# Optimization experiments

Hardware: AMD Instinct MI355X
Metric: run time of the kernel (lower is better)

The kernel has to match this reference:

```python
import jax, jax.numpy as jnp
import numpy as np

FP8_MAX = 448.0   # max normal of float8_e4m3fn
BLOCK = 128       # block_size
EPS = 1e-12


def setup_inputs() -> dict:
    key = jax.random.key(0)
    k1, k2 = jax.random.split(key)
    M, K, N = 8192, 2048, 2048  # tokens, in_features, out_features
    x = jax.random.normal(k1, (M, K), dtype=jnp.float32)
    # Build an fp8 blockwise-quantized weight (as the module stores it):
    w = jax.random.normal(k2, (N, K), dtype=jnp.float32) * 0.02
    wb = w.reshape(N // BLOCK, BLOCK, K // BLOCK, BLOCK)
    amax = jnp.max(jnp.abs(wb), axis=(1, 3))                      # [Nb, Kb]
    w_scale = jnp.maximum(amax, EPS) / FP8_MAX                    # fp32 per-block scale
    w_q = (wb / w_scale[:, None, :, None]).astype(jnp.float8_e4m3fn)
    weight = w_q.reshape(N, K)                                    # fp8 [N, K]
    return {"x": x, "weight": weight, "w_scale": w_scale}


def reference(x, weight, w_scale):
    M, K = x.shape
    N = weight.shape[0]
    # --- fp8_blockwise_act_quant: per (1, BLOCK) block along last dim ---
    xb = x.reshape(M, K // BLOCK, BLOCK)
    amax = jnp.max(jnp.abs(xb), axis=-1)                          # [M, Kb]
    x_scale = jnp.maximum(amax, EPS) / FP8_MAX                    # [M, Kb]
    x_q = (xb / x_scale[:, :, None]).astype(jnp.float8_e4m3fn).astype(jnp.float32)
    # --- blockwise_fp8_gemm: y[m,n] = sum_kb (xq_blk . wq_blk) * xs[m,kb] * ws[nb,kb]
    # Scales factor per-block, so dequantize then a single GEMM is exactly equivalent.
    x_deq = (x_q * x_scale[:, :, None]).reshape(M, K)             # [M, K]
    ws_full = jnp.repeat(jnp.repeat(w_scale, BLOCK, axis=0), BLOCK, axis=1)  # [N, K]
    w_deq = weight.astype(jnp.float32) * ws_full                  # [N, K]
    y = x_deq @ w_deq.T                                           # [M, N]
    return y
```

## Files before the change

kernel.cpp:

```cpp
#include <hip/hip_runtime.h>
#include <cstdint>
#include <cstddef>

#define MDIM 8192
#define KDIM 2048
#define NDIM 2048
#define QBLK 128
#define KB   (KDIM / QBLK)
#define NB   (NDIM / QBLK)

typedef float floatx4 __attribute__((ext_vector_type(4)));
typedef int   int4v   __attribute__((ext_vector_type(4)));
typedef int   int8v   __attribute__((ext_vector_type(8)));

#define AS1 __attribute__((address_space(1)))
#define AS3 __attribute__((address_space(3)))

__device__ inline float e4m3_rne(float q) {
    float aq = fabsf(q);
    float r;
    if (aq < 0.015625f) {
        r = rintf(aq * 512.0f) * 0.001953125f;
    } else {
        unsigned u = __float_as_uint(aq);
        unsigned rem = u & 0xFFFFFu;
        unsigned base = u & ~0xFFFFFu;
        unsigned inc = (rem > 0x80000u || (rem == 0x80000u && (u & 0x100000u))) ? 0x100000u : 0u;
        r = __uint_as_float(base + inc);
    }
    return q < 0.0f ? -r : r;
}

__device__ inline unsigned e4m3_encode(float r) {
    unsigned u = __float_as_uint(r);
    unsigned s = (u >> 24) & 0x80u;
    float a = fabsf(r);
    if (a < 0.015625f) return s | (unsigned)(a * 512.0f + 0.25f);
    unsigned e = ((u >> 23) & 0xFFu) - 120u;
    unsigned m = (u >> 20) & 7u;
    return s | (e << 3) | m;
}

__device__ inline float e4m3_decode(unsigned b) {
    unsigned s = b >> 7, e = (b >> 3) & 0xFu, m = b & 7u;
    float v;
    if (e == 0) v = (float)m * 0.001953125f;
    else        v = __uint_as_float((e + 120u) << 23) * (float)(8 + m) * 0.125f;
    return s ? -v : v;
}

__device__ inline int is_expbyte(unsigned b) {
    unsigned e = b & 0x7Fu;
    return (e >= 0x3Bu && e <= 0x43u) || e == 0x00u;
}

#define XQ_OFF  0
#define WQ_OFF  ((size_t)MDIM * KDIM)
#define XS_OFF  (WQ_OFF + (size_t)NDIM * KDIM)
#define FL_OFF  (XS_OFF + (size_t)MDIM * KB * 4)

#define QXB ((MDIM * KB) / 8)
#define DWB ((NDIM * KDIM / 8) / 256)

__global__ __launch_bounds__(256) void prep_kernel(const float* __restrict__ x,
                                                   const void* __restrict__ wq,
                                                   unsigned char* __restrict__ xq,
                                                   unsigned char* __restrict__ wq8,
                                                   float* __restrict__ xs,
                                                   int* __restrict__ flag) {
    const int tid = threadIdx.x;
    if (blockIdx.x == 0 && tid == 0) *flag = 0;

    if (blockIdx.x < QXB) {
        const int g = tid >> 5;
        const int l = tid & 31;
        const size_t bi = (size_t)blockIdx.x * 8 + g;
        const size_t base = bi << 7;

        const float4 v = *(const float4*)(x + base + (size_t)l * 4);
        float a = fmaxf(fmaxf(fabsf(v.x), fabsf(v.y)), fmaxf(fabsf(v.z), fabsf(v.w)));
        a = fmaxf(a, __shfl_xor(a, 1));
        a = fmaxf(a, __shfl_xor(a, 2));
        a = fmaxf(a, __shfl_xor(a, 4));
        a = fmaxf(a, __shfl_xor(a, 8));
        a = fmaxf(a, __shfl_xor(a, 16));

        const float scale = fmaxf(a, 1e-12f) / 448.0f;
        if (l == 0) xs[bi] = scale;

        const float q0 = v.x / scale, q1 = v.y / scale;
        const float q2 = v.z / scale, q3 = v.w / scale;
        int w = __builtin_amdgcn_cvt_pk_fp8_f32(q0, q1, 0, false);
        w = __builtin_amdgcn_cvt_pk_fp8_f32(q2, q3, w, true);
        *(unsigned*)(xq + base + (size_t)l * 4) = (unsigned)w;
    } else {
        const int lane = tid & 63;
        const unsigned pw = ((const unsigned*)wq)[lane];
        const unsigned long long m3 = __ballot(is_expbyte((pw >> 24) & 0xFFu));
        const unsigned long long m1 = __ballot(((pw >> 8) & 0xFFu) == 0u);
        const int f = (__popcll(m3) >= 56) ? ((__popcll(m1) >= 56) ? 2 : 1) : 0;

        const size_t idx = (size_t)(blockIdx.x - QXB) * 256 + tid;
        const size_t off = idx * 8;

        unsigned lo, hi;
        if (f == 2) {
            const float4* p = (const float4*)((const float*)wq + off);
            const float4 a = p[0], b = p[1];
            lo = e4m3_encode(a.x) | (e4m3_encode(a.y) << 8) | (e4m3_encode(a.z) << 16) | (e4m3_encode(a.w) << 24);
            hi = e4m3_encode(b.x) | (e4m3_encode(b.y) << 8) | (e4m3_encode(b.z) << 16) | (e4m3_encode(b.w) << 24);
        } else if (f == 1) {
            const ushort4 h0 = *(const ushort4*)((const unsigned short*)wq + off);
            const ushort4 h1 = *(((const ushort4*)((const unsigned short*)wq + off)) + 1);
            lo = e4m3_encode(__uint_as_float((unsigned)h0.x << 16))
               | (e4m3_encode(__uint_as_float((unsigned)h0.y << 16)) << 8)
               | (e4m3_encode(__uint_as_float((unsigned)h0.z << 16)) << 16)
               | (e4m3_encode(__uint_as_float((unsigned)h0.w << 16)) << 24);
            hi = e4m3_encode(__uint_as_float((unsigned)h1.x << 16))
               | (e4m3_encode(__uint_as_float((unsigned)h1.y << 16)) << 8)
               | (e4m3_encode(__uint_as_float((unsigned)h1.z << 16)) << 16)
               | (e4m3_encode(__uint_as_float((unsigned)h1.w << 16)) << 24);
        } else {
            const uint2 d = *(const uint2*)((const unsigned char*)wq + off);
            lo = d.x; hi = d.y;
        }
        *(uint2*)(wq8 + off) = make_uint2(lo, hi);
    }
}

__global__ __launch_bounds__(512, 2) void gemm_mx_kernel(const unsigned char* __restrict__ Aq,
                                                         const unsigned char* __restrict__ Bq,
                                                         const float* __restrict__ xs,
                                                         const float* __restrict__ wsc,
                                                         float* __restrict__ C) {
    __shared__ unsigned char sA[2][256 * 128];
    __shared__ unsigned char sB[2][256 * 128];
    __shared__ float sxs[KB][256];

    const int tid  = threadIdx.x;
    const int wave = tid >> 6;
    const int lane = tid & 63;
    const int lrow = lane & 15;
    const int lk   = lane >> 4;
    const int wml  = (wave >> 2) * 128;
    const int wnl  = (wave & 3) * 64;

    const int bid = blockIdx.x;
    const int lid = ((bid & 7) << 5) + (bid >> 3);
    const int m0  = (lid >> 3) * 256;
    const int n0  = (lid & 7) * 256;
    const int nb  = (n0 + wnl) >> 7;

    const int srow = tid >> 3;
    const int gck  = (tid & 7) ^ (srow & 7);
    const unsigned char* agp = Aq + (size_t)(m0 + srow) * KDIM + gck * 16;
    const unsigned char* bgp = Bq + (size_t)(n0 + srow) * KDIM + gck * 16;

#define STAGE(buf, kb_) do {                                                          \
    const size_t koff_ = (size_t)(kb_) * QBLK;                                        \
    _Pragma("unroll")                                                                 \
    for (int it = 0; it < 4; ++it)                                                    \
        __builtin_amdgcn_global_load_lds(                                             \
            (const AS1 void*)(agp + (size_t)(it * 64) * KDIM + koff_),                \
            (AS3 void*)(&sA[buf][0] + tid * 16 + it * 8192), 16, 0, 0);               \
    _Pragma("unroll")                                                                 \
    for (int it = 0; it < 4; ++it)                                                    \
        __builtin_amdgcn_global_load_lds(                                             \
            (const AS1 void*)(bgp + (size_t)(it * 64) * KDIM + koff_),                \
            (AS3 void*)(&sB[buf][0] + tid * 16 + it * 8192), 16, 0, 0);               \
} while (0)

    STAGE(0, 0);
    if (tid < 256) {
        const float4* xp = (const float4*)(xs + (size_t)(m0 + tid) * KB);
#pragma unroll
        for (int q = 0; q < 4; ++q) {
            const float4 v = xp[q];
            sxs[q * 4 + 0][tid] = v.x;
            sxs[q * 4 + 1][tid] = v.y;
            sxs[q * 4 + 2][tid] = v.z;
            sxs[q * 4 + 3][tid] = v.w;
        }
    }
    __syncthreads();

    floatx4 acc[8][4] = {};
    const floatx4 zero = {0.f, 0.f, 0.f, 0.f};

    for (int kb = 0; kb < KB; ++kb) {
        const int cur = kb & 1;
        if (kb + 1 < KB) STAGE(cur ^ 1, kb + 1);

        int8v bf[4];
#pragma unroll
        for (int j = 0; j < 4; ++j) {
            const int Rb = wnl + j * 16 + lrow;
            const int d0 = (lk * 2) ^ (Rb & 7);
            const int d1 = (lk * 2 + 1) ^ (Rb & 7);
            int4v blo = *(const int4v*)(&sB[cur][0] + Rb * 128 + d0 * 16);
            int4v bhi = *(const int4v*)(&sB[cur][0] + Rb * 128 + d1 * 16);
            bf[j] = __builtin_shufflevector(blo, bhi, 0, 1, 2, 3, 4, 5, 6, 7);
        }
        const float wsk = wsc[nb * KB + kb];

#pragma unroll
        for (int i = 0; i < 8; ++i) {
            const int Ra = wml + i * 16 + lrow;
            const int c0 = (lk * 2) ^ (Ra & 7);
            const int c1 = (lk * 2 + 1) ^ (Ra & 7);
            int4v alo = *(const int4v*)(&sA[cur][0] + Ra * 128 + c0 * 16);
            int4v ahi = *(const int4v*)(&sA[cur][0] + Ra * 128 + c1 * 16);
            int8v af = __builtin_shufflevector(alo, ahi, 0, 1, 2, 3, 4, 5, 6, 7);

            const float4 xv = *(const float4*)(&sxs[kb][wml + i * 16 + lk * 4]);
            const float cs0 = xv.x * wsk, cs1 = xv.y * wsk;
            const float cs2 = xv.z * wsk, cs3 = xv.w * wsk;

#pragma unroll
            for (int j = 0; j < 4; ++j) {
                floatx4 blk = __builtin_amdgcn_mfma_scale_f32_16x16x128_f8f6f4(
                    af, bf[j], zero, 0, 0, 0, 0x7F7F7F7F, 0, 0x7F7F7F7F);
                acc[i][j][0] += cs0 * blk[0];
                acc[i][j][1] += cs1 * blk[1];
                acc[i][j][2] += cs2 * blk[2];
                acc[i][j][3] += cs3 * blk[3];
            }
        }
        __syncthreads();
    }
#undef STAGE

#pragma unroll
    for (int i = 0; i < 8; ++i) {
        const int row0 = m0 + wml + i * 16 + lk * 4;
#pragma unroll
        for (int r = 0; r < 4; ++r) {
            float* cp = C + (size_t)(row0 + r) * NDIM + n0 + wnl + lrow;
#pragma unroll
            for (int j = 0; j < 4; ++j)
                cp[j * 16] = acc[i][j][r];
        }
    }
}

__global__ __launch_bounds__(256) void check_kernel(const unsigned char* __restrict__ xq,
                                                    const unsigned char* __restrict__ wq8,
                                                    const float* __restrict__ xs,
                                                    const float* __restrict__ wsc,
                                                    const float* __restrict__ y,
                                                    int* __restrict__ flag) {
    const int s = blockIdx.x;
    const int m = (s * 1237 + 11) & (MDIM - 1);
    const int n = (s * 389 + 7) & (NDIM - 1);
    const int tid = threadIdx.x;
    const int k0 = tid * 8;
    const int kb = k0 >> 7;

    const unsigned char* xp = xq + (size_t)m * KDIM + k0;
    const unsigned char* wp = wq8 + (size_t)n * KDIM + k0;
    float dot = 0.f;
#pragma unroll
    for (int i = 0; i < 8; ++i)
        dot += e4m3_decode(xp[i]) * e4m3_decode(wp[i]);
    float part = dot * xs[m * KB + kb] * wsc[(n >> 7) * KB + kb];

#pragma unroll
    for (int o = 32; o > 0; o >>= 1) part += __shfl_down(part, o);
    __shared__ float wsum[4];
    if ((tid & 63) == 0) wsum[tid >> 6] = part;
    __syncthreads();
    if (tid == 0) {
        const float tot = wsum[0] + wsum[1] + wsum[2] + wsum[3];
        const float d = tot - y[(size_t)m * NDIM + n];
        if (!(fabsf(d) <= 0.05f)) atomicOr(flag, 1);
    }
}

__global__ __launch_bounds__(256, 2) void gemm_fb_kernel(const unsigned char* __restrict__ Aq,
                                                         const unsigned char* __restrict__ Bq,
                                                         const float* __restrict__ xs,
                                                         const float* __restrict__ wsc,
                                                         float* __restrict__ C,
                                                         const int* __restrict__ flag) {
    if (*flag == 0) return;

    __shared__ unsigned char sA[128 * 128];
    __shared__ unsigned char sB[128 * 128];

    const int tid  = threadIdx.x;
    const int wave = tid >> 6;
    const int lane = tid & 63;
    const int lrow = lane & 15;
    const int lk   = lane >> 4;
    const int wm   = (wave & 1) * 64;
    const int wn   = (wave >> 1) * 64;
    const int m0   = blockIdx.y * 128;
    const int n0   = blockIdx.x * 128;
    const int nb   = n0 >> 7;

    const int srow = tid >> 3;
    const int gck  = (tid & 7) ^ (srow & 7);
    const unsigned char* agp = Aq + (size_t)(m0 + srow) * KDIM + gck * 16;
    const unsigned char* bgp = Bq + (size_t)(n0 + srow) * KDIM + gck * 16;

    floatx4 acc[4][4] = {};

    for (int kb = 0; kb < KB; ++kb) {
        const size_t koff = (size_t)kb * QBLK;
        __syncthreads();
#pragma unroll
        for (int it = 0; it < 4; ++it)
            __builtin_amdgcn_global_load_lds(
                (const AS1 void*)(agp + (size_t)(it * 32) * KDIM + koff),
                (AS3 void*)(sA + tid * 16 + it * 4096), 16, 0, 0);
#pragma unroll
        for (int it = 0; it < 4; ++it)
            __builtin_amdgcn_global_load_lds(
                (const AS1 void*)(bgp + (size_t)(it * 32) * KDIM + koff),
                (AS3 void*)(sB + tid * 16 + it * 4096), 16, 0, 0);
        __syncthreads();

        floatx4 blk[4][4] = {};
#pragma unroll
        for (int ks = 0; ks < 4; ++ks) {
            long a8[4], b8[4];
            const int lc = ks * 2 + (lk >> 1);
            const int bo = (lk & 1) * 8;
#pragma unroll
            for (int i = 0; i < 4; ++i) {
                const int Ra = wm + i * 16 + lrow;
                a8[i] = *(const long*)(sA + Ra * 128 + (lc ^ (Ra & 7)) * 16 + bo);
                const int Rb = wn + i * 16 + lrow;
                b8[i] = *(const long*)(sB + Rb * 128 + (lc ^ (Rb & 7)) * 16 + bo);
            }
#pragma unroll
            for (int i = 0; i < 4; ++i)
#pragma unroll
                for (int j = 0; j < 4; ++j)
                    blk[i][j] = __builtin_amdgcn_mfma_f32_16x16x32_fp8_fp8(a8[i], b8[j], blk[i][j], 0, 0, 0);
        }

        const float wsk = wsc[nb * KB + kb];
#pragma unroll
        for (int i = 0; i < 4; ++i) {
            float cs[4];
#pragma unroll
            for (int r = 0; r < 4; ++r)
                cs[r] = xs[(size_t)(m0 + wm + i * 16 + lk * 4 + r) * KB + kb] * wsk;
#pragma unroll
            for (int j = 0; j < 4; ++j)
#pragma unroll
                for (int r = 0; r < 4; ++r)
                    acc[i][j][r] += cs[r] * blk[i][j][r];
        }
    }

#pragma unroll
    for (int i = 0; i < 4; ++i) {
        const int row0 = m0 + wm + i * 16 + lk * 4;
#pragma unroll
        for (int r = 0; r < 4; ++r) {
            float* cp = C + (size_t)(row0 + r) * NDIM + n0 + wn + lrow;
#pragma unroll
            for (int j = 0; j < 4; ++j)
                cp[j * 16] = acc[i][j][r];
        }
    }
}

extern "C" void kernel_launch(void* const* d_in, const int* in_sizes, int n_in,
                              void* d_out, int out_size, void* d_ws, size_t ws_size,
                              hipStream_t stream) {
    const float* x      = (const float*)d_in[0];
    const void* wq      = d_in[1];
    const float* wscale = (const float*)d_in[2];
    float* y            = (float*)d_out;

    unsigned char* xq  = (unsigned char*)d_ws + XQ_OFF;
    unsigned char* wq8 = (unsigned char*)d_ws + WQ_OFF;
    float* xs          = (float*)((unsigned char*)d_ws + XS_OFF);
    int* flag          = (int*)((unsigned char*)d_ws + FL_OFF);

    prep_kernel<<<QXB + DWB, 256, 0, stream>>>(x, wq, xq, wq8, xs, flag);
    gemm_mx_kernel<<<(MDIM / 256) * (NDIM / 256), 512, 0, stream>>>(xq, wq8, xs, wscale, y);
    check_kernel<<<64, 256, 0, stream>>>(xq, wq8, xs, wscale, y, flag);
    gemm_fb_kernel<<<dim3(NDIM / 128, MDIM / 128), 256, 0, stream>>>(xq, wq8, xs, wscale, y, flag);
}
```

Measured before the change: 174.1 us.

## Restructure fp8 GEMM into 256x128 tiles with interleaved load/MFMA phases

The GEMM now uses 256x128 output tiles with 8 waves each owning a 64x64 subtile. It also splits every K-block iteration into four phases that interleave the global-to-LDS loads for the next block with MFMA work, using explicit vmcnt waits, barriers and setprio. Per-block weight scales are staged in LDS, and the activation quantization prep processes 8 elements per thread. The goal is better overlap of memory and matrix ops and a better fit of the grid to the CUs, at the cost of more barriers and hand-tuned wait counts that are fragile to get right.

```diff
diff --git a/kernel.cpp b/kernel.cpp
--- a/kernel.cpp
+++ b/kernel.cpp
@@ -59,7 +59,7 @@
 #define XS_OFF  (WQ_OFF + (size_t)NDIM * KDIM)
 #define FL_OFF  (XS_OFF + (size_t)MDIM * KB * 4)
 
-#define QXB ((MDIM * KB) / 8)
+#define QXB ((MDIM * KB) / 16)
 #define DWB ((NDIM * KDIM / 8) / 256)
 
 __global__ __launch_bounds__(256) void prep_kernel(const float* __restrict__ x,
@@ -72,27 +72,30 @@
     if (blockIdx.x == 0 && tid == 0) *flag = 0;
 
     if (blockIdx.x < QXB) {
-        const int g = tid >> 5;
-        const int l = tid & 31;
-        const size_t bi = (size_t)blockIdx.x * 8 + g;
+        const int g = tid >> 4;
+        const int l = tid & 15;
+        const size_t bi = (size_t)blockIdx.x * 16 + g;
         const size_t base = bi << 7;
 
-        const float4 v = *(const float4*)(x + base + (size_t)l * 4);
-        float a = fmaxf(fmaxf(fabsf(v.x), fabsf(v.y)), fmaxf(fabsf(v.z), fabsf(v.w)));
+        const float4* xp = (const float4*)(x + base + (size_t)l * 8);
+        const float4 v0 = xp[0], v1 = xp[1];
+        float a = fmaxf(fmaxf(fmaxf(fabsf(v0.x), fabsf(v0.y)), fmaxf(fabsf(v0.z), fabsf(v0.w))),
+                        fmaxf(fmaxf(fabsf(v1.x), fabsf(v1.y)), fmaxf(fabsf(v1.z), fabsf(v1.w))));
         a = fmaxf(a, __shfl_xor(a, 1));
         a = fmaxf(a, __shfl_xor(a, 2));
         a = fmaxf(a, __shfl_xor(a, 4));
         a = fmaxf(a, __shfl_xor(a, 8));
-        a = fmaxf(a, __shfl_xor(a, 16));
 
         const float scale = fmaxf(a, 1e-12f) / 448.0f;
         if (l == 0) xs[bi] = scale;
 
-        const float q0 = v.x / scale, q1 = v.y / scale;
-        const float q2 = v.z / scale, q3 = v.w / scale;
-        int w = __builtin_amdgcn_cvt_pk_fp8_f32(q0, q1, 0, false);
-        w = __builtin_amdgcn_cvt_pk_fp8_f32(q2, q3, w, true);
-        *(unsigned*)(xq + base + (size_t)l * 4) = (unsigned)w;
+        const float q0 = v0.x / scale, q1 = v0.y / scale, q2 = v0.z / scale, q3 = v0.w / scale;
+        const float q4 = v1.x / scale, q5 = v1.y / scale, q6 = v1.z / scale, q7 = v1.w / scale;
+        int w0 = __builtin_amdgcn_cvt_pk_fp8_f32(q0, q1, 0, false);
+        w0 = __builtin_amdgcn_cvt_pk_fp8_f32(q2, q3, w0, true);
+        int w1 = __builtin_amdgcn_cvt_pk_fp8_f32(q4, q5, 0, false);
+        w1 = __builtin_amdgcn_cvt_pk_fp8_f32(q6, q7, w1, true);
+        *(uint2*)(xq + base + (size_t)l * 8) = make_uint2((unsigned)w0, (unsigned)w1);
     } else {
         const int lane = tid & 63;
         const unsigned pw = ((const unsigned*)wq)[lane];
@@ -134,43 +137,33 @@
                                                          const float* __restrict__ wsc,
                                                          float* __restrict__ C) {
     __shared__ unsigned char sA[2][256 * 128];
-    __shared__ unsigned char sB[2][256 * 128];
+    __shared__ unsigned char sB[2][128 * 128];
     __shared__ float sxs[KB][256];
+    __shared__ float swk[KB];
 
     const int tid  = threadIdx.x;
     const int wave = tid >> 6;
     const int lane = tid & 63;
     const int lrow = lane & 15;
     const int lk   = lane >> 4;
-    const int wml  = (wave >> 2) * 128;
-    const int wnl  = (wave & 3) * 64;
-
-    const int bid = blockIdx.x;
-    const int lid = ((bid & 7) << 5) + (bid >> 3);
-    const int m0  = (lid >> 3) * 256;
-    const int n0  = (lid & 7) * 256;
-    const int nb  = (n0 + wnl) >> 7;
-
-    const int srow = tid >> 3;
-    const int gck  = (tid & 7) ^ (srow & 7);
-    const unsigned char* agp = Aq + (size_t)(m0 + srow) * KDIM + gck * 16;
-    const unsigned char* bgp = Bq + (size_t)(n0 + srow) * KDIM + gck * 16;
-
-#define STAGE(buf, kb_) do {                                                          \
-    const size_t koff_ = (size_t)(kb_) * QBLK;                                        \
-    _Pragma("unroll")                                                                 \
-    for (int it = 0; it < 4; ++it)                                                    \
-        __builtin_amdgcn_global_load_lds(                                             \
-            (const AS1 void*)(agp + (size_t)(it * 64) * KDIM + koff_),                \
-            (AS3 void*)(&sA[buf][0] + tid * 16 + it * 8192), 16, 0, 0);               \
-    _Pragma("unroll")                                                                 \
-    for (int it = 0; it < 4; ++it)                                                    \
-        __builtin_amdgcn_global_load_lds(                                             \
-            (const AS1 void*)(bgp + (size_t)(it * 64) * KDIM + koff_),                \
-            (AS3 void*)(&sB[buf][0] + tid * 16 + it * 8192), 16, 0, 0);               \
-} while (0)
-
-    STAGE(0, 0);
+    const int lk4  = lk * 4;
+    const int wm64 = (wave >> 1) * 64;
+    const int wn64 = (wave & 1) * 64;
+
+    const int bid   = blockIdx.x;
+    const int lid   = ((bid & 7) << 6) | (bid >> 3);
+    const int m0    = (lid >> 4) * 256;
+    const int ntile = lid & 15;
+    const int n0    = ntile * 128;
+
+    const int rbase = 64 * (tid >> 8) + ((tid >> 3) & 31);
+    const int gck   = (tid & 7) ^ ((tid >> 3) & 7);
+    const unsigned char* agp = Aq + (size_t)(m0 + rbase) * KDIM + (size_t)gck * 16;
+    const unsigned char* bgp = Bq + (size_t)(n0 + rbase) * KDIM + (size_t)gck * 16;
+    const int ldsT = rbase * 128 + (tid & 7) * 16;
+
+#define GL(SRC, DST) __builtin_amdgcn_global_load_lds((const AS1 void*)(SRC), (AS3 void*)(DST), 16, 0, 0)
+
     if (tid < 256) {
         const float4* xp = (const float4*)(xs + (size_t)(m0 + tid) * KB);
 #pragma unroll
@@ -182,60 +175,147 @@
             sxs[q * 4 + 3][tid] = v.w;
         }
     }
-    __syncthreads();
-
-    floatx4 acc[8][4] = {};
+    if (tid < KB) swk[tid] = wsc[ntile * KB + tid];
+
+    GL(agp,                              &sA[0][0] + ldsT);
+    GL(agp + (size_t)128 * KDIM,         &sA[0][0] + 16384 + ldsT);
+    GL(bgp,                              &sB[0][0] + ldsT);
+    GL(bgp + (size_t)32 * KDIM,          &sB[0][0] + 4096 + ldsT);
+    GL(agp + (size_t)32 * KDIM,          &sA[0][0] + 4096 + ldsT);
+    GL(agp + (size_t)160 * KDIM,         &sA[0][0] + 20480 + ldsT);
+
+    asm volatile("s_waitcnt vmcnt(3) lgkmcnt(0)" ::: "memory");
+    asm volatile("s_barrier" ::: "memory");
+
+    floatx4 acc[4][4] = {};
     const floatx4 zero = {0.f, 0.f, 0.f, 0.f};
-
-    for (int kb = 0; kb < KB; ++kb) {
-        const int cur = kb & 1;
-        if (kb + 1 < KB) STAGE(cur ^ 1, kb + 1);
-
-        int8v bf[4];
-#pragma unroll
-        for (int j = 0; j < 4; ++j) {
-            const int Rb = wnl + j * 16 + lrow;
-            const int d0 = (lk * 2) ^ (Rb & 7);
-            const int d1 = (lk * 2 + 1) ^ (Rb & 7);
-            int4v blo = *(const int4v*)(&sB[cur][0] + Rb * 128 + d0 * 16);
-            int4v bhi = *(const int4v*)(&sB[cur][0] + Rb * 128 + d1 * 16);
-            bf[j] = __builtin_shufflevector(blo, bhi, 0, 1, 2, 3, 4, 5, 6, 7);
-        }
-        const float wsk = wsc[nb * KB + kb];
-
-#pragma unroll
-        for (int i = 0; i < 8; ++i) {
-            const int Ra = wml + i * 16 + lrow;
-            const int c0 = (lk * 2) ^ (Ra & 7);
-            const int c1 = (lk * 2 + 1) ^ (Ra & 7);
-            int4v alo = *(const int4v*)(&sA[cur][0] + Ra * 128 + c0 * 16);
-            int4v ahi = *(const int4v*)(&sA[cur][0] + Ra * 128 + c1 * 16);
-            int8v af = __builtin_shufflevector(alo, ahi, 0, 1, 2, 3, 4, 5, 6, 7);
-
-            const float4 xv = *(const float4*)(&sxs[kb][wml + i * 16 + lk * 4]);
-            const float cs0 = xv.x * wsk, cs1 = xv.y * wsk;
-            const float cs2 = xv.z * wsk, cs3 = xv.w * wsk;
-
-#pragma unroll
-            for (int j = 0; j < 4; ++j) {
-                floatx4 blk = __builtin_amdgcn_mfma_scale_f32_16x16x128_f8f6f4(
-                    af, bf[j], zero, 0, 0, 0, 0x7F7F7F7F, 0, 0x7F7F7F7F);
-                acc[i][j][0] += cs0 * blk[0];
-                acc[i][j][1] += cs1 * blk[1];
-                acc[i][j][2] += cs2 * blk[2];
-                acc[i][j][3] += cs3 * blk[3];
-            }
-        }
-        __syncthreads();
-    }
-#undef STAGE
-
-#pragma unroll
-    for (int i = 0; i < 8; ++i) {
-        const int row0 = m0 + wml + i * 16 + lk * 4;
+    int8v af0, af1, bfa, bfb;
+    floatx4 cs0, cs1;
+
+#define FRAG(dst, basep, ROW) do {                                              \
+    const int _r = (ROW);                                                       \
+    const unsigned char* _p = (basep) + _r * 128;                               \
+    const int _c0 = (lk * 2) ^ (_r & 7);                                        \
+    ((int4v*)&(dst))[0] = *(const int4v*)(_p + _c0 * 16);                       \
+    ((int4v*)&(dst))[1] = *(const int4v*)(_p + (_c0 ^ 1) * 16);                 \
+} while (0)
+
+#define MM(I, J, AF, BF, CS) do {                                               \
+    floatx4 _blk = __builtin_amdgcn_mfma_scale_f32_16x16x128_f8f6f4(            \
+        AF, BF, zero, 0, 0, 0, 0x7F7F7F7F, 0, 0x7F7F7F7F);                      \
+    acc[I][J] += (CS) * _blk;                                                   \
+} while (0)
+
+    const int arA = wm64 + lrow;
+    const int arB = wn64 + lrow;
+
+    for (int t = 0; t < KB - 1; ++t) {
+        const int cur = t & 1;
+        const unsigned char* sAc = &sA[cur][0];
+        const unsigned char* sBc = &sB[cur][0];
+        unsigned char* sAn = &sA[cur ^ 1][0];
+        unsigned char* sBn = &sB[cur ^ 1][0];
+        const size_t koff2 = (size_t)(t + 1) * QBLK;
+        const float wsk = swk[t];
+
+        FRAG(af0, sAc, arA);
+        FRAG(af1, sAc, arA + 16);
+        FRAG(bfa, sBc, arB);
+        FRAG(bfb, sBc, arB + 16);
+        cs0 = (*(const floatx4*)&sxs[t][wm64 + lk4]) * wsk;
+        cs1 = (*(const floatx4*)&sxs[t][wm64 + 16 + lk4]) * wsk;
+        GL(agp + koff2,                       sAn + ldsT);
+        GL(agp + (size_t)128 * KDIM + koff2,  sAn + 16384 + ldsT);
+        asm volatile("s_barrier" ::: "memory");
+        __builtin_amdgcn_s_setprio(1);
+        MM(0, 0, af0, bfa, cs0); MM(0, 1, af0, bfb, cs0);
+        MM(1, 0, af1, bfa, cs1); MM(1, 1, af1, bfb, cs1);
+        __builtin_amdgcn_s_setprio(0);
+        asm volatile("s_waitcnt vmcnt(4)" ::: "memory");
+        asm volatile("s_barrier" ::: "memory");
+
+        FRAG(bfa, sBc, arB + 32);
+        FRAG(bfb, sBc, arB + 48);
+        GL(bgp + koff2,                       sBn + ldsT);
+        GL(bgp + (size_t)32 * KDIM + koff2,   sBn + 4096 + ldsT);
+        asm volatile("s_barrier" ::: "memory");
+        __builtin_amdgcn_s_setprio(1);
+        MM(0, 2, af0, bfa, cs0); MM(0, 3, af0, bfb, cs0);
+        MM(1, 2, af1, bfa, cs1); MM(1, 3, af1, bfb, cs1);
+        __builtin_amdgcn_s_setprio(0);
+        asm volatile("s_waitcnt vmcnt(4)" ::: "memory");
+        asm volatile("s_barrier" ::: "memory");
+
+        FRAG(af0, sAc, arA + 32);
+        FRAG(af1, sAc, arA + 48);
+        cs0 = (*(const floatx4*)&sxs[t][wm64 + 32 + lk4]) * wsk;
+        cs1 = (*(const floatx4*)&sxs[t][wm64 + 48 + lk4]) * wsk;
+        GL(agp + (size_t)32 * KDIM + koff2,   sAn + 4096 + ldsT);
+        GL(agp + (size_t)160 * KDIM + koff2,  sAn + 20480 + ldsT);
+        asm volatile("s_barrier" ::: "memory");
+        __builtin_amdgcn_s_setprio(1);
+        MM(2, 2, af0, bfa, cs0); MM(2, 3, af0, bfb, cs0);
+        MM(3, 2, af1, bfa, cs1); MM(3, 3, af1, bfb, cs1);
+        __builtin_amdgcn_s_setprio(0);
+        asm volatile("s_barrier" ::: "memory");
+
+        FRAG(bfa, sBc, arB);
+        FRAG(bfb, sBc, arB + 16);
+        asm volatile("s_barrier" ::: "memory");
+        __builtin_amdgcn_s_setprio(1);
+        MM(2, 0, af0, bfa, cs0); MM(2, 1, af0, bfb, cs0);
+        MM(3, 0, af1, bfa, cs1); MM(3, 1, af1, bfb, cs1);
+        __builtin_amdgcn_s_setprio(0);
+        asm volatile("s_waitcnt vmcnt(3)" ::: "memory");
+        asm volatile("s_barrier" ::: "memory");
+    }
+
+    {
+        const int t = KB - 1;
+        const unsigned char* sAc = &sA[1][0];
+        const unsigned char* sBc = &sB[1][0];
+        const float wsk = swk[t];
+
+        FRAG(af0, sAc, arA);
+        FRAG(af1, sAc, arA + 16);
+        FRAG(bfa, sBc, arB);
+        FRAG(bfb, sBc, arB + 16);
+        cs0 = (*(const floatx4*)&sxs[t][wm64 + lk4]) * wsk;
+        cs1 = (*(const floatx4*)&sxs[t][wm64 + 16 + lk4]) * wsk;
+        MM(0, 0, af0, bfa, cs0); MM(0, 1, af0, bfb, cs0);
+        MM(1, 0, af1, bfa, cs1); MM(1, 1, af1, bfb, cs1);
+        asm volatile("s_waitcnt vmcnt(2)" ::: "memory");
+        asm volatile("s_barrier" ::: "memory");
+
+        FRAG(bfa, sBc, arB + 32);
+        FRAG(bfb, sBc, arB + 48);
+        MM(0, 2, af0, bfa, cs0); MM(0, 3, af0, bfb, cs0);
+        MM(1, 2, af1, bfa, cs1); MM(1, 3, af1, bfb, cs1);
+        asm volatile("s_waitcnt vmcnt(0)" ::: "memory");
+        asm volatile("s_barrier" ::: "memory");
+
+        FRAG(af0, sAc, arA + 32);
+        FRAG(af1, sAc, arA + 48);
+        cs0 = (*(const floatx4*)&sxs[t][wm64 + 32 + lk4]) * wsk;
+        cs1 = (*(const floatx4*)&sxs[t][wm64 + 48 + lk4]) * wsk;
+        MM(2, 2, af0, bfa, cs0); MM(2, 3, af0, bfb, cs0);
+        MM(3, 2, af1, bfa, cs1); MM(3, 3, af1, bfb, cs1);
+
+        FRAG(bfa, sBc, arB);
+        FRAG(bfb, sBc, arB + 16);
+        MM(2, 0, af0, bfa, cs0); MM(2, 1, af0, bfb, cs0);
+        MM(3, 0, af1, bfa, cs1); MM(3, 1, af1, bfb, cs1);
+    }
+#undef FRAG
+#undef MM
+#undef GL
+
+#pragma unroll
+    for (int i = 0; i < 4; ++i) {
+        const int row0 = m0 + wm64 + i * 16 + lk4;
 #pragma unroll
         for (int r = 0; r < 4; ++r) {
-            float* cp = C + (size_t)(row0 + r) * NDIM + n0 + wnl + lrow;
+            float* cp = C + (size_t)(row0 + r) * NDIM + n0 + wn64 + lrow;
 #pragma unroll
             for (int j = 0; j < 4; ++j)
                 cp[j * 16] = acc[i][j][r];
@@ -382,7 +462,7 @@
     int* flag          = (int*)((unsigned char*)d_ws + FL_OFF);
 
     prep_kernel<<<QXB + DWB, 256, 0, stream>>>(x, wq, xq, wq8, xs, flag);
-    gemm_mx_kernel<<<(MDIM / 256) * (NDIM / 256), 512, 0, stream>>>(xq, wq8, xs, wscale, y);
+    gemm_mx_kernel<<<(MDIM / 256) * (NDIM / 128), 512, 0, stream>>>(xq, wq8, xs, wscale, y);
     check_kernel<<<64, 256, 0, stream>>>(xq, wq8, xs, wscale, y, flag);
     gemm_fb_kernel<<<dim3(NDIM / 128, MDIM / 128), 256, 0, stream>>>(xq, wq8, xs, wscale, y, flag);
 }
```

Result: slower. 182.0 us (+4.5%).
